# Kernel tuning notes

Measured on AMD Instinct MI355X. Metric: run time of the kernel, lower is better.

## Reference

```python
import jax, jax.numpy as jnp
import numpy as np

N_NODES = 30000
N_EDGES = 480000
C_IN = 256
D_HEAD = 64   # out_channels
N_HEADS = 4
M_FEAT = 30   # nb_random_features
K_GUMBEL = 10
TAU = 0.25


def _linear_init(key, out_f, in_f):
    s = 1.0 / np.sqrt(in_f)
    k1, k2 = jax.random.split(key)
    w = jax.random.uniform(k1, (out_f, in_f), minval=-s, maxval=s, dtype=jnp.float32)
    b = jax.random.uniform(k2, (out_f,), minval=-s, maxval=s, dtype=jnp.float32)
    return w, b


def setup_inputs() -> dict:
    key = jax.random.key(0)
    ks = jax.random.split(key, 8)
    z = jax.random.normal(ks[0], (1, N_NODES, C_IN), dtype=jnp.float32)
    edge_index = jax.random.randint(ks[1], (2, N_EDGES), 0, N_NODES)
    # Gumbel(0,1)/tau noise, matching torch's (-Exp(1).log())/tau
    u = jax.random.uniform(ks[2], (N_NODES, 1, N_HEADS, K_GUMBEL), dtype=jnp.float32,
                           minval=1e-8, maxval=1.0)
    gumbels = -jnp.log(-jnp.log(u)) / TAU
    # Performer orthogonal random-feature projection matrix [M, D]
    rng = np.random.default_rng(0)
    q, _ = np.linalg.qr(rng.standard_normal((D_HEAD, D_HEAD)))
    q = q.T[:M_FEAT]
    mult = np.linalg.norm(rng.standard_normal((M_FEAT, D_HEAD)), axis=1)
    proj = jnp.asarray(np.diag(mult) @ q, dtype=jnp.float32)
    Wq_w, Wq_b = _linear_init(ks[3], N_HEADS * D_HEAD, C_IN)
    Wk_w, Wk_b = _linear_init(ks[4], N_HEADS * D_HEAD, C_IN)
    Wv_w, Wv_b = _linear_init(ks[5], N_HEADS * D_HEAD, C_IN)
    Wo_w, Wo_b = _linear_init(ks[6], D_HEAD, N_HEADS * D_HEAD)
    b = jnp.full((1, N_HEADS), 0.1, dtype=jnp.float32)  # rb_order=1, sigmoid init
    tau = jnp.float32(TAU)
    return {"z": z, "edge_index": edge_index, "tau": tau, "gumbels": gumbels,
            "proj": proj, "Wq_w": Wq_w, "Wq_b": Wq_b, "Wk_w": Wk_w, "Wk_b": Wk_b,
            "Wv_w": Wv_w, "Wv_b": Wv_b, "Wo_w": Wo_w, "Wo_b": Wo_b, "b": b}


def _softmax_kernel_feats(data, proj, is_query):
    # data: [B, N, H, D] -> phi(data): [B, N, H, M]
    dn = 1.0 / jnp.sqrt(jnp.sqrt(jnp.float32(data.shape[-1])))
    data = data * dn
    ratio = 1.0 / jnp.sqrt(jnp.float32(proj.shape[0]))
    dash = jnp.einsum('bnhd,md->bnhm', data, proj)
    diag = jnp.sum(data * data, axis=-1, keepdims=True) * 0.5
    if is_query:
        stab = jnp.max(dash, axis=-1, keepdims=True)
    else:
        stab = jnp.max(dash, axis=(1, 3), keepdims=True)
    return ratio * (jnp.exp(dash - diag - stab) + 1e-6)


def reference(z, edge_index, tau, gumbels, proj, Wq_w, Wq_b, Wk_w, Wk_b,
              Wv_w, Wv_b, Wo_w, Wo_b, b):
    B, N, _ = z.shape
    M, D = proj.shape
    H = Wq_w.shape[0] // D
    query = (z @ Wq_w.T + Wq_b).reshape(B, N, H, D)
    key = (z @ Wk_w.T + Wk_b).reshape(B, N, H, D)
    value = (z @ Wv_w.T + Wv_b).reshape(B, N, H, D)

    inv_sqrt_tau = 1.0 / jnp.sqrt(tau)
    qp = jnp.transpose(_softmax_kernel_feats(query * inv_sqrt_tau, proj, True), (1, 0, 2, 3))   # [N,B,H,M]
    kp = jnp.transpose(_softmax_kernel_feats(key * inv_sqrt_tau, proj, False), (1, 0, 2, 3))    # [N,B,H,M]
    v = jnp.transpose(value, (1, 0, 2, 3))                                                       # [N,B,H,D]

    # Gumbel-perturbed key features: [N,B,H,K,M]
    kg = kp[:, :, :, None, :] * jnp.exp(gumbels)[..., None]
    kvs = jnp.einsum('nbhkm,nbhd->bhkmd', kg, v)
    z_num = jnp.einsum('nbhm,bhkmd->nbhkd', qp, kvs)      # [N,B,H,K,D]
    z_den = jnp.einsum('nbhm,bhkm->nbhk', qp, kg.sum(axis=0))
    z_out = jnp.transpose(jnp.mean(z_num / z_den[..., None], axis=3), (1, 0, 2, 3))  # [B,N,H,D]

    # edge attention weights (for link loss)
    start, end = edge_index[0], edge_index[1]
    edge_num = jnp.transpose(jnp.einsum('ebhm,ebhm->ebh', qp[end], kp[start]), (1, 0, 2))  # [B,E,H]
    attn_norm = jnp.einsum('nbhm,bhm->nbh', qp, kp.sum(axis=0))
    edge_dem = jnp.transpose(attn_norm[end], (1, 0, 2))
    A_weight = edge_num / edge_dem

    # relational bias (rb_order=1, sigmoid), degree-normalized sparse conv over value
    ones_e = jnp.ones(start.shape[0], dtype=jnp.float32)
    d_in = jax.ops.segment_sum(ones_e, end, num_segments=N)
    d_out = jax.ops.segment_sum(ones_e, start, num_segments=N)
    edge_w = jax.nn.sigmoid(b[0])[None, :] * jnp.sqrt((1.0 / d_in[end]) * (1.0 / d_out[start]))[:, None]  # [E,H]
    conv = jax.vmap(lambda vb: jax.ops.segment_sum(vb[start] * edge_w[:, :, None], end,
                                                   num_segments=N))(value)
    z_out = z_out + conv

    z_next = z_out.reshape(B, N, H * D) @ Wo_w.T + Wo_b  # [B,N,D]

    d_norm = 1.0 / d_in[end]
    link_loss = jnp.mean(jnp.log(A_weight) * d_norm[None, :, None])
    return z_next, link_loss
```

## Files before the change

### kernel.cpp

```cpp
#include <hip/hip_runtime.h>
#include <hip/hip_bf16.h>

#define NN 30000
#define NE 480000
#define NH 4
#define DH 64
#define MF 30
#define KG 10
#define RATIO 0.18257418583505536f
#define DNRM  0.35355339059327373f

#define P_WF    0
#define P_BF    196608
#define P_WOF   197376
#define P_WOBF  213760
#define P_BBF   213824
#define P_PROJ  213828
#define P_TAU   215748
#define P_TOTAL 215749

typedef unsigned short u16;
typedef unsigned int   u32;
typedef __attribute__((ext_vector_type(8))) short bf16x8;
typedef __attribute__((ext_vector_type(4))) float f32x4;

__device__ __forceinline__ float u2f(u16 u) { return __uint_as_float(((u32)u) << 16); }
__device__ __forceinline__ u16  f2bf(float f) {
    u32 x = __float_as_uint(f);
    return (u16)((x + 0x7FFFu + ((x >> 16) & 1u)) >> 16);
}
__device__ __forceinline__ u32  encf(float f) { u32 u = __float_as_uint(f); return (u & 0x80000000u) ? ~u : (u | 0x80000000u); }
__device__ __forceinline__ float decf(u32 u)  { return (u & 0x80000000u) ? __uint_as_float(u & 0x7FFFFFFFu) : __uint_as_float(~u); }

__global__ void k_detect(const u16* __restrict__ z, int* __restrict__ flag) {
    if (threadIdx.x == 0 && blockIdx.x == 0) {
        int bad = 0;
        for (int i = 0; i < 256; i += 2) {
            u16 u = z[i];
            int e = (u >> 7) & 0xFF;
            if (u != 0 && !(e >= 100 && e <= 140)) bad++;
        }
        *flag = (bad > 16) ? 1 : 0;
    }
}

__global__ __launch_bounds__(256) void k_cvt_params(
    const void* Wq, const void* Wk, const void* Wv,
    const void* bq, const void* bk, const void* bv,
    const void* Wo, const void* Wob, const void* bb, const void* proj,
    const void* taup, float* __restrict__ params, const int* __restrict__ flag)
{
    int i = blockIdx.x * 256 + threadIdx.x;
    if (i >= P_TOTAL) return;
    int f = *flag;
    if (i == P_TAU) {
        float v = f ? ((const float*)taup)[0] : u2f(((const u16*)taup)[0]);
        if (!(v > 1e-6f && v < 1e6f)) {
            float ff = ((const float*)taup)[0];
            v = (ff > 1e-6f && ff < 1e6f) ? ff : 0.25f;
        }
        params[i] = v;
        return;
    }
    const void* src; int j;
    if      (i < 65536)  { src = Wq;  j = i; }
    else if (i < 131072) { src = Wk;  j = i - 65536; }
    else if (i < 196608) { src = Wv;  j = i - 131072; }
    else if (i < 196864) { src = bq;  j = i - 196608; }
    else if (i < 197120) { src = bk;  j = i - 196864; }
    else if (i < 197376) { src = bv;  j = i - 197120; }
    else if (i < 213760) { src = Wo;  j = i - 197376; }
    else if (i < 213824) { src = Wob; j = i - 213760; }
    else if (i < 213828) { src = bb;  j = i - 213824; }
    else                 { src = proj; j = i - P_PROJ; }
    params[i] = f ? ((const float*)src)[j] : u2f(((const u16*)src)[j]);
}

__global__ __launch_bounds__(256) void k_cvt_w(const float* __restrict__ params,
                                               u16* __restrict__ Wh, u16* __restrict__ Wl)
{
    int i = blockIdx.x * 256 + threadIdx.x;
    float x = params[P_WF + i];
    u16 h = f2bf(x);
    Wh[i] = h;
    Wl[i] = f2bf(x - u2f(h));
}

__global__ __launch_bounds__(256) void k_deg(const int* __restrict__ ei, int* __restrict__ din, int* __restrict__ dout) {
    int e = blockIdx.x * 256 + threadIdx.x;
    if (e >= NE) return;
    atomicAdd(&dout[ei[e]], 1);
    atomicAdd(&din[ei[NE + e]], 1);
}

__global__ __launch_bounds__(256) void k_off(const int* __restrict__ din, int* __restrict__ offn, int* __restrict__ counter) {
    __shared__ int s[256];
    __shared__ int base;
    int tid = threadIdx.x;
    int n = blockIdx.x * 256 + tid;
    int v = (n < NN) ? din[n] : 0;
    s[tid] = v;
    __syncthreads();
    for (int o = 1; o < 256; o <<= 1) {
        int t = (tid >= o) ? s[tid - o] : 0;
        __syncthreads();
        s[tid] += t;
        __syncthreads();
    }
    if (tid == 255) base = atomicAdd(counter, s[255]);
    __syncthreads();
    if (n < NN) offn[n] = base + s[tid] - v;
}

__global__ __launch_bounds__(256) void k_fill(const int* __restrict__ ei, const int* __restrict__ offn,
                                              int* __restrict__ fill, int* __restrict__ csr,
                                              const int* __restrict__ din, const int* __restrict__ dout,
                                              float* __restrict__ wedge) {
    int e = blockIdx.x * 256 + threadIdx.x;
    if (e >= NE) return;
    int s = ei[e], t = ei[NE + e];
    int pos = offn[t] + atomicAdd(&fill[t], 1);
    csr[pos] = s;
    wedge[pos] = rsqrtf((float)din[t] * (float)dout[s]);
}

__global__ __launch_bounds__(256) void k_gemm_feat(
    const void* __restrict__ zv, const float* __restrict__ params, const int* __restrict__ flag,
    const u16* __restrict__ Wh, const u16* __restrict__ Wl,
    u16* __restrict__ V16, float* __restrict__ qp, u16* __restrict__ qp16,
    float* __restrict__ dashK, float* __restrict__ diagK, u32* __restrict__ stab)
{
    __shared__ __align__(16) char AsH[64 * 512];
    __shared__ __align__(16) char AsL[64 * 512];
    __shared__ __align__(16) char BsH[2][64 * 128];
    __shared__ __align__(16) char BsL[2][64 * 128];
    __shared__ float tile[64 * 68];
    __shared__ float projL[30 * 65];
    __shared__ u32 smaxL;

    const int tid = threadIdx.x;
    const int bm = blockIdx.x * 64;
    const int f32 = *flag;
    const int wave = tid >> 6, lane = tid & 63;
    const int wm = wave >> 1, wn = wave & 1;
    const int sr = tid >> 2;
    const int sc = (tid & 3) * 16;

    {
        int zrow = bm + sr;
        if (f32) {
            for (int k0 = 0; k0 < 256; k0 += 64) {
                float x[16];
                if (zrow < NN) {
                    const float4* zp = (const float4*)((const float*)zv + (size_t)zrow * 256 + k0 + sc);
                    #pragma unroll
                    for (int q4 = 0; q4 < 4; ++q4) {
                        float4 v = zp[q4];
                        x[q4 * 4 + 0] = v.x; x[q4 * 4 + 1] = v.y;
                        x[q4 * 4 + 2] = v.z; x[q4 * 4 + 3] = v.w;
                    }
                } else {
                    #pragma unroll
                    for (int j = 0; j < 16; ++j) x[j] = 0.f;
                }
                #pragma unroll
                for (int j8 = 0; j8 < 2; ++j8) {
                    u32 hw[4], lw[4];
                    #pragma unroll
                    for (int p = 0; p < 4; ++p) {
                        float a = x[j8 * 8 + 2 * p], b2 = x[j8 * 8 + 2 * p + 1];
                        u16 ha = f2bf(a), hb = f2bf(b2);
                        hw[p] = (u32)ha | ((u32)hb << 16);
                        u16 la = f2bf(a - u2f(ha)), lb = f2bf(b2 - u2f(hb));
                        lw[p] = (u32)la | ((u32)lb << 16);
                    }
                    int byt = sr * 512 + (((k0 + sc + j8 * 8) * 2) ^ ((sr & 7) << 4));
                    *(uint4*)(AsH + byt) = make_uint4(hw[0], hw[1], hw[2], hw[3]);
                    *(uint4*)(AsL + byt) = make_uint4(lw[0], lw[1], lw[2], lw[3]);
                }
            }
        } else {
            for (int k0 = 0; k0 < 256; k0 += 64) {
                uint4 v0 = make_uint4(0, 0, 0, 0), v1 = v0;
                if (zrow < NN) {
                    const uint4* zp = (const uint4*)((const u16*)zv + (size_t)zrow * 256 + k0 + sc);
                    v0 = zp[0]; v1 = zp[1];
                }
                int byt0 = sr * 512 + (((k0 + sc + 0) * 2) ^ ((sr & 7) << 4));
                int byt1 = sr * 512 + (((k0 + sc + 8) * 2) ^ ((sr & 7) << 4));
                *(uint4*)(AsH + byt0) = v0;
                *(uint4*)(AsH + byt1) = v1;
            }
        }
    }
    for (int i2 = tid; i2 < MF * DH; i2 += 256) projL[(i2 >> 6) * 65 + (i2 & 63)] = params[P_PROJ + i2];

    const float* bfv = params + P_BF;
    float scale = DNRM * rsqrtf(params[P_TAU]);

    for (int bny = 0; bny < 12; ++bny) {
        const int bn = bny * 64;
        f32x4 acc[2][2] = {};
        for (int k0c = 0; k0c < 4; ++k0c) {
            const int k0 = k0c * 64;
            const int p = k0c & 1;
            {
                int byt0 = sr * 128 + (((sc + 0) * 2) ^ ((sr & 7) << 4));
                int byt1 = sr * 128 + (((sc + 8) * 2) ^ ((sr & 7) << 4));
                const uint4* wh4 = (const uint4*)(Wh + (size_t)(bn + sr) * 256 + k0 + sc);
                *(uint4*)(BsH[p] + byt0) = wh4[0];
                *(uint4*)(BsH[p] + byt1) = wh4[1];
                if (f32) {
                    const uint4* wl4 = (const uint4*)(Wl + (size_t)(bn + sr) * 256 + k0 + sc);
                    *(uint4*)(BsL[p] + byt0) = wl4[0];
                    *(uint4*)(BsL[p] + byt1) = wl4[1];
                }
            }
            __syncthreads();
            #pragma unroll
            for (int kk = 0; kk < 2; ++kk) {
                const int kbA = (k0 + kk * 32 + ((lane >> 4) * 8)) * 2;
                const int kbB = (kk * 32 + ((lane >> 4) * 8)) * 2;
                bf16x8 ah[2], bh[2], al[2], bl[2];
                #pragma unroll
                for (int i = 0; i < 2; ++i) {
                    int ar = 32 * wm + 16 * i + (lane & 15);
                    int ab = ar * 512 + (kbA ^ ((ar & 7) << 4));
                    ah[i] = *(const bf16x8*)(AsH + ab);
                    int br = 32 * wn + 16 * i + (lane & 15);
                    int bb2 = br * 128 + (kbB ^ ((br & 7) << 4));
                    bh[i] = *(const bf16x8*)(BsH[p] + bb2);
                    if (f32) {
                        al[i] = *(const bf16x8*)(AsL + ab);
                        bl[i] = *(const bf16x8*)(BsL[p] + bb2);
                    }
                }
                #pragma unroll
                for (int i = 0; i < 2; ++i)
                    #pragma unroll
                    for (int nf = 0; nf < 2; ++nf) {
                        acc[i][nf] = __builtin_amdgcn_mfma_f32_16x16x32_bf16(ah[i], bh[nf], acc[i][nf], 0, 0, 0);
                        if (f32) {
                            acc[i][nf] = __builtin_amdgcn_mfma_f32_16x16x32_bf16(ah[i], bl[nf], acc[i][nf], 0, 0, 0);
                            acc[i][nf] = __builtin_amdgcn_mfma_f32_16x16x32_bf16(al[i], bh[nf], acc[i][nf], 0, 0, 0);
                        }
                    }
            }
        }
        if (bny >= 8) {
            #pragma unroll
            for (int i = 0; i < 2; ++i)
                #pragma unroll
                for (int nf = 0; nf < 2; ++nf) {
                    int col = 32 * wn + 16 * nf + (lane & 15);
                    float bias = bfv[bn + col];
                    #pragma unroll
                    for (int r2 = 0; r2 < 4; ++r2) {
                        int row = 32 * wm + 16 * i + ((lane >> 4) * 4) + r2;
                        tile[row * 68 + col] = acc[i][nf][r2] + bias;
                    }
                }
            __syncthreads();
            for (int i2 = tid; i2 < 4096; i2 += 256) {
                int row = i2 >> 6, col = i2 & 63;
                int nrow = bm + row;
                if (nrow < NN) V16[(size_t)nrow * 256 + (bn - 512) + col] = f2bf(tile[row * 68 + col]);
            }
            continue;
        }

        if (tid == 0) smaxL = 0u;
        #pragma unroll
        for (int i = 0; i < 2; ++i)
            #pragma unroll
            for (int nf = 0; nf < 2; ++nf) {
                int col = 32 * wn + 16 * nf + (lane & 15);
                float bias = bfv[bn + col];
                #pragma unroll
                for (int r2 = 0; r2 < 4; ++r2) {
                    int row = 32 * wm + 16 * i + ((lane >> 4) * 4) + r2;
                    tile[row * 68 + col] = (acc[i][nf][r2] + bias) * scale;
                }
            }
        __syncthreads();

        int r = tid >> 2, q = tid & 3;
        int n = bm + r;
        const float* trow = tile + r * 68;
        float dp = 0.f;
        #pragma unroll
        for (int d = q * 16; d < q * 16 + 16; ++d) dp += trow[d] * trow[d];
        dp += __shfl_xor(dp, 1);
        dp += __shfl_xor(dp, 2);
        float diag = dp * 0.5f;

        float dm[8];
        int nm = 0;
        float lmax = -3.0e38f;
        for (int m = q; m < MF; m += 4) {
            float s = 0.f;
            #pragma unroll
            for (int d = 0; d < DH; ++d) s += trow[d] * projL[m * 65 + d];
            dm[nm++] = s;
            lmax = fmaxf(lmax, s);
        }
        float mx = fmaxf(lmax, __shfl_xor(lmax, 1));
        mx = fmaxf(mx, __shfl_xor(mx, 2));

        if (bny < 4) {
            int h = bny;
            if (n < NN) {
                float* o = qp + ((size_t)n * NH + h) * MF;
                u16* o16 = qp16 + ((size_t)n * NH + h) * 32;
                nm = 0;
                for (int m = q; m < MF; m += 4) {
                    float v = RATIO * (expf(dm[nm++] - diag - mx) + 1e-6f);
                    o[m] = v;
                    o16[m] = f2bf(v);
                }
                if (q == 0) { o16[30] = 0; o16[31] = 0; }
            }
        } else {
            int h = bny - 4;
            if (n < NN) {
                float* o = dashK + ((size_t)n * NH + h) * MF;
                nm = 0;
                for (int m = q; m < MF; m += 4) o[m] = dm[nm++];
                if (q == 0) {
                    diagK[(size_t)n * NH + h] = diag;
                    atomicMax(&smaxL, encf(mx));
                }
            }
            __syncthreads();
            if (tid == 0) atomicMax(&stab[h], smaxL);
        }
    }
}

__global__ __launch_bounds__(256) void k_kp(float* __restrict__ kp, const float* __restrict__ diagK,
                                            const u32* __restrict__ stab, float* __restrict__ kpsum,
                                            u16* __restrict__ kp16)
{
    __shared__ float part[NH * MF];
    __shared__ float stabf[4];
    int tid = threadIdx.x;
    if (tid < NH * MF) part[tid] = 0.f;
    if (tid >= 128 && tid < 132) stabf[tid - 128] = decf(stab[tid - 128]);
    __syncthreads();
    int base = blockIdx.x * 64 * MF;
    for (int i = tid; i < 64 * MF; i += 256) {
        int row = blockIdx.x * 64 + i / MF;
        int m = i - (i / MF) * MF;
        int h = row & 3;
        float v = RATIO * (expf(kp[base + i] - diagK[row] - stabf[h]) + 1e-6f);
        kp[base + i] = v;
        kp16[(size_t)row * 32 + m] = f2bf(v);
        atomicAdd(&part[h * MF + m], v);
    }
    if (tid < 64) {
        int row = blockIdx.x * 64 + tid;
        kp16[(size_t)row * 32 + 30] = 0;
        kp16[(size_t)row * 32 + 31] = 0;
    }
    __syncthreads();
    if (tid < NH * MF) atomicAdd(&kpsum[tid], part[tid]);
}

__global__ __launch_bounds__(256) void k_an(const float* __restrict__ qp, const float* __restrict__ kpsum,
                                            float* __restrict__ an)
{
    __shared__ float kps[NH * MF];
    int tid = threadIdx.x;
    if (tid < NH * MF) kps[tid] = kpsum[tid];
    __syncthreads();
    int idx = blockIdx.x * 256 + tid;
    if (idx >= NN * NH) return;
    int h = idx & 3;
    const float* q = qp + (size_t)idx * MF;
    float s = 0.f;
    #pragma unroll
    for (int m = 0; m < MF; ++m) s += q[m] * kps[h * MF + m];
    an[idx] = s;
}

#define KVS_CHUNKS 50
#define KVS_NPB (NN / KVS_CHUNKS)
__global__ __launch_bounds__(512) void k_kvs(const float* __restrict__ kp, const void* __restrict__ gum,
                                             const u16* __restrict__ V16, const int* __restrict__ flag,
                                             float* __restrict__ Pkvs, float* __restrict__ Pksum)
{
    __shared__ __align__(16) char kgT[320 * 128];
    __shared__ __align__(16) char VT[64 * 128];
    __shared__ float kpT[64][31];
    __shared__ float egT[64][10];
    const int tid = threadIdx.x;
    const int h = blockIdx.y;
    const int chunk = blockIdx.x;
    const int n0 = chunk * KVS_NPB;
    const int f32 = *flag;
    const int wave = tid >> 6, lane = tid & 63;

    float ksacc[5] = {0.f, 0.f, 0.f, 0.f, 0.f};
    f32x4 acc[10] = {};

    for (int t0 = 0; t0 < KVS_NPB; t0 += 64) {
        __syncthreads();
        for (int i = tid; i < 64 * MF; i += 512) {
            int n = i / MF, m = i - (i / MF) * MF;
            kpT[n][m] = (t0 + n < KVS_NPB) ? kp[(size_t)(n0 + t0 + n) * (NH * MF) + h * MF + m] : 0.f;
        }
        for (int i = tid; i < 64 * KG; i += 512) {
            int n = i / KG, k = i - (i / KG) * KG;
            float e = 0.f;
            if (t0 + n < KVS_NPB) {
                size_t gofs = (size_t)(n0 + t0 + n) * (NH * KG) + h * KG + k;
                float g = f32 ? ((const float*)gum)[gofs] : u2f(((const u16*)gum)[gofs]);
                e = expf(g);
            }
            egT[n][k] = e;
        }
        for (int i = tid; i < 64 * 16; i += 512) {
            int n = i >> 4, dq = (i & 15) * 4;
            u32 v0 = 0, v1 = 0;
            if (t0 + n < KVS_NPB) {
                uint2 vv = *(const uint2*)(V16 + (size_t)(n0 + t0 + n) * 256 + h * 64 + dq);
                v0 = vv.x; v1 = vv.y;
            }
            #pragma unroll
            for (int j = 0; j < 4; ++j) {
                u16 val = (u16)(((j < 2) ? v0 : v1) >> ((j & 1) * 16));
                int d = dq + j;
                *(u16*)(VT + d * 128 + ((n * 2) ^ ((d & 7) << 4))) = val;
            }
        }
        __syncthreads();
        #pragma unroll
        for (int it = 0; it < 5; ++it) {
            int idx = tid + it * 512;
            int row = idx >> 3, nc = idx & 7;
            u32 w_[4] = {0u, 0u, 0u, 0u};
            if (row < 300) {
                int k = row / MF, m = row - (row / MF) * MF;
                float s = 0.f;
                #pragma unroll
                for (int p = 0; p < 4; ++p) {
                    int na = nc * 8 + 2 * p, nb = na + 1;
                    u16 ha = f2bf(kpT[na][m] * egT[na][k]);
                    u16 hb = f2bf(kpT[nb][m] * egT[nb][k]);
                    w_[p] = (u32)ha | ((u32)hb << 16);
                    s += u2f(ha) + u2f(hb);
                }
                ksacc[it] += s;
            }
            *(uint4*)(kgT + row * 128 + ((nc * 16) ^ ((row & 7) << 4))) = make_uint4(w_[0], w_[1], w_[2], w_[3]);
        }
        __syncthreads();
        #pragma unroll
        for (int kk = 0; kk < 2; ++kk) {
            const int kb = (kk * 32 + ((lane >> 4) * 8)) * 2;
            #pragma unroll
            for (int i = 0; i < 10; ++i) {
                int ct = wave * 10 + i;
                int kt = ct >> 2, dt = ct & 3;
                int ar = kt * 16 + (lane & 15);
                bf16x8 a = *(const bf16x8*)(kgT + ar * 128 + (kb ^ ((ar & 7) << 4)));
                int br = dt * 16 + (lane & 15);
                bf16x8 b = *(const bf16x8*)(VT + br * 128 + (kb ^ ((br & 7) << 4)));
                acc[i] = __builtin_amdgcn_mfma_f32_16x16x32_bf16(a, b, acc[i], 0, 0, 0);
            }
        }
    }
    #pragma unroll
    for (int i = 0; i < 10; ++i) {
        int ct = wave * 10 + i;
        int kt = ct >> 2, dt = ct & 3;
        int col = dt * 16 + (lane & 15);
        #pragma unroll
        for (int r = 0; r < 4; ++r) {
            int row = kt * 16 + ((lane >> 4) * 4) + r;
            if (row < 300)
                Pkvs[(((size_t)chunk * NH + h) * 300 + row) * 64 + col] = acc[i][r];
        }
    }
    #pragma unroll
    for (int it = 0; it < 5; ++it) {
        float v = ksacc[it];
        v += __shfl_xor(v, 1);
        v += __shfl_xor(v, 2);
        v += __shfl_xor(v, 4);
        int row = (tid + it * 512) >> 3;
        if ((tid & 7) == 0 && row < 300)
            Pksum[chunk * 1200 + h * 300 + row] = v;
    }
}

__global__ __launch_bounds__(256) void k_reduce(const float* __restrict__ Pkvs, const float* __restrict__ Pksum,
                                                float* __restrict__ kvs, float* __restrict__ ksum)
{
    int i = blockIdx.x * 256 + threadIdx.x;
    if (i < NH * KG * MF * DH) {
        float s = 0.f;
        for (int c = 0; c < KVS_CHUNKS; ++c) s += Pkvs[(size_t)c * (NH * 300 * 64) + i];
        kvs[i] = s;
    } else if (i < NH * KG * MF * DH + NH * KG * MF) {
        int j = i - NH * KG * MF * DH;
        float s = 0.f;
        for (int c = 0; c < KVS_CHUNKS; ++c) s += Pksum[c * 1200 + j];
        ksum[j] = s;
    }
}

__global__ __launch_bounds__(256) void k_edge(const int* __restrict__ ei,
                                              const u16* __restrict__ qp16, const u16* __restrict__ kp16,
                                              const float* __restrict__ an,
                                              const int* __restrict__ din, float* __restrict__ lossp)
{
    __shared__ float ls[64];
    int tid = threadIdx.x;
    int eg = tid >> 2, h = tid & 3;
    int e = blockIdx.x * 64 + eg;
    int s = ei[e], t = ei[NE + e];
    const uint4* qv = (const uint4*)(qp16 + ((size_t)t * NH + h) * 32);
    const uint4* kv = (const uint4*)(kp16 + ((size_t)s * NH + h) * 32);
    float num = 0.f;
    #pragma unroll
    for (int c = 0; c < 4; ++c) {
        uint4 a = qv[c], b = kv[c];
        num += u2f((u16)(a.x & 0xFFFF)) * u2f((u16)(b.x & 0xFFFF))
             + u2f((u16)(a.x >> 16))    * u2f((u16)(b.x >> 16))
             + u2f((u16)(a.y & 0xFFFF)) * u2f((u16)(b.y & 0xFFFF))
             + u2f((u16)(a.y >> 16))    * u2f((u16)(b.y >> 16))
             + u2f((u16)(a.z & 0xFFFF)) * u2f((u16)(b.z & 0xFFFF))
             + u2f((u16)(a.z >> 16))    * u2f((u16)(b.z >> 16))
             + u2f((u16)(a.w & 0xFFFF)) * u2f((u16)(b.w & 0xFFFF))
             + u2f((u16)(a.w >> 16))    * u2f((u16)(b.w >> 16));
    }
    float term = logf(num / an[(size_t)t * NH + h]);
    term += __shfl_xor(term, 1);
    term += __shfl_xor(term, 2);
    if (h == 0) ls[eg] = term / (float)din[t];
    __syncthreads();
    if (tid < 64) {
        float v = ls[tid];
        #pragma unroll
        for (int o = 32; o > 0; o >>= 1) v += __shfl_xor(v, o);
        if (tid == 0) atomicAdd(&lossp[blockIdx.x & 1023], v);
    }
}

#define AT_NT 48
__global__ __launch_bounds__(256) void k_attn(
    const float* __restrict__ qp, const float* __restrict__ kvs, const float* __restrict__ ksum,
    u16* __restrict__ zatt)
{
    __shared__ float qpTf[3][NH * 484];
    __shared__ u32   kvbuf[NH * 964];
    __shared__ float rdenL[3][16 * NH * KG];
    u16*   kvL16 = (u16*)kvbuf;
    float* ksL   = (float*)kvbuf;
    int tid = threadIdx.x;
    int n0 = blockIdx.x * AT_NT;

    for (int i = tid; i < AT_NT * NH * MF; i += 256) {
        int j48 = i / (NH * MF); int r = i - j48 * (NH * MF);
        int h = r / MF; int m = r - h * MF;
        qpTf[j48 >> 4][h * 484 + m * 16 + (j48 & 15)] = qp[(size_t)(n0 + j48) * (NH * MF) + r];
    }
    for (int i = tid; i < NH * KG * MF; i += 256) ksL[i] = ksum[i];
    __syncthreads();
    for (int i = tid; i < AT_NT * NH * KG; i += 256) {
        int j48 = i / (NH * KG); int r = i - j48 * (NH * KG);
        int h = r / KG;
        int sub = j48 >> 4, j = j48 & 15;
        float s = 0.f;
        #pragma unroll
        for (int m = 0; m < MF; ++m) s += qpTf[sub][h * 484 + m * 16 + j] * ksL[r * MF + m];
        rdenL[sub][j * (NH * KG) + r] = 1.0f / s;
    }

    const int h  = tid >> 6;
    const int jg = (tid >> 4) & 3;
    const int dg = tid & 15;
    float acc[3][4][4] = {};
    for (int k = 0; k < KG; ++k) {
        __syncthreads();
        for (int i = tid; i < NH * MF * DH; i += 256) {
            int hh = i / (MF * DH); int r = i - hh * (MF * DH);
            kvL16[hh * 1928 + r] = f2bf(kvs[((size_t)(hh * 10 + k) * MF) * DH + r]);
        }
        __syncthreads();
        float ps[3][4][4] = {};
        const u16* kb = kvL16 + h * 1928 + dg * 4;
        const float* qb0 = qpTf[0] + h * 484 + jg * 4;
        const float* qb1 = qpTf[1] + h * 484 + jg * 4;
        const float* qb2 = qpTf[2] + h * 484 + jg * 4;
        #pragma unroll
        for (int m = 0; m < MF; ++m) {
            ushort4 bu = *(const ushort4*)(kb + m * 64);
            float4 b = make_float4(u2f(bu.x), u2f(bu.y), u2f(bu.z), u2f(bu.w));
            float4 a0 = *(const float4*)(qb0 + m * 16);
            float4 a1 = *(const float4*)(qb1 + m * 16);
            float4 a2 = *(const float4*)(qb2 + m * 16);
            ps[0][0][0] += a0.x * b.x; ps[0][0][1] += a0.x * b.y; ps[0][0][2] += a0.x * b.z; ps[0][0][3] += a0.x * b.w;
            ps[0][1][0] += a0.y * b.x; ps[0][1][1] += a0.y * b.y; ps[0][1][2] += a0.y * b.z; ps[0][1][3] += a0.y * b.w;
            ps[0][2][0] += a0.z * b.x; ps[0][2][1] += a0.z * b.y; ps[0][2][2] += a0.z * b.z; ps[0][2][3] += a0.z * b.w;
            ps[0][3][0] += a0.w * b.x; ps[0][3][1] += a0.w * b.y; ps[0][3][2] += a0.w * b.z; ps[0][3][3] += a0.w * b.w;
            ps[1][0][0] += a1.x * b.x; ps[1][0][1] += a1.x * b.y; ps[1][0][2] += a1.x * b.z; ps[1][0][3] += a1.x * b.w;
            ps[1][1][0] += a1.y * b.x; ps[1][1][1] += a1.y * b.y; ps[1][1][2] += a1.y * b.z; ps[1][1][3] += a1.y * b.w;
            ps[1][2][0] += a1.z * b.x; ps[1][2][1] += a1.z * b.y; ps[1][2][2] += a1.z * b.z; ps[1][2][3] += a1.z * b.w;
            ps[1][3][0] += a1.w * b.x; ps[1][3][1] += a1.w * b.y; ps[1][3][2] += a1.w * b.z; ps[1][3][3] += a1.w * b.w;
            ps[2][0][0] += a2.x * b.x; ps[2][0][1] += a2.x * b.y; ps[2][0][2] += a2.x * b.z; ps[2][0][3] += a2.x * b.w;
            ps[2][1][0] += a2.y * b.x; ps[2][1][1] += a2.y * b.y; ps[2][1][2] += a2.y * b.z; ps[2][1][3] += a2.y * b.w;
            ps[2][2][0] += a2.z * b.x; ps[2][2][1] += a2.z * b.y; ps[2][2][2] += a2.z * b.z; ps[2][2][3] += a2.z * b.w;
            ps[2][3][0] += a2.w * b.x; ps[2][3][1] += a2.w * b.y; ps[2][3][2] += a2.w * b.z; ps[2][3][3] += a2.w * b.w;
        }
        #pragma unroll
        for (int sub = 0; sub < 3; ++sub)
            #pragma unroll
            for (int j4 = 0; j4 < 4; ++j4) {
                float rd = rdenL[sub][(jg * 4 + j4) * (NH * KG) + h * KG + k];
                #pragma unroll
                for (int d4 = 0; d4 < 4; ++d4) acc[sub][j4][d4] += ps[sub][j4][d4] * rd;
            }
    }
    #pragma unroll
    for (int sub = 0; sub < 3; ++sub)
        #pragma unroll
        for (int j4 = 0; j4 < 4; ++j4) {
            int n = n0 + sub * 16 + jg * 4 + j4;
            #pragma unroll
            for (int d4 = 0; d4 < 4; ++d4)
                zatt[(size_t)n * 256 + h * 64 + dg * 4 + d4] = f2bf(acc[sub][j4][d4] * (1.0f / KG));
        }
}

__global__ __launch_bounds__(256) void k_gather(
    const u16* __restrict__ zatt, const u16* __restrict__ V16,
    const int* __restrict__ csr, const float* __restrict__ wedge,
    const int* __restrict__ offn, const int* __restrict__ din,
    const float* __restrict__ params, u16* __restrict__ pre)
{
    int tid = threadIdx.x;
    int w = tid >> 6, l = tid & 63;
    int n = blockIdx.x * 4 + w;
    float sigb = 1.f / (1.f + expf(-params[P_BBF + (l >> 4)]));
    int dn = din[n], o0 = offn[n];
    float c0 = 0.f, c1 = 0.f, c2 = 0.f, c3 = 0.f;
    for (int t0 = 0; t0 < dn; t0 += 64) {
        int cnt = min(64, dn - t0);
        int myIdx = 0; float myW = 0.f;
        if (l < cnt) { myIdx = csr[o0 + t0 + l]; myW = wedge[o0 + t0 + l]; }
        int j = 0;
        for (; j + 7 < cnt; j += 8) {
            int   s0 = __shfl(myIdx, j),     s1 = __shfl(myIdx, j + 1);
            int   s2 = __shfl(myIdx, j + 2), s3 = __shfl(myIdx, j + 3);
            int   s4 = __shfl(myIdx, j + 4), s5 = __shfl(myIdx, j + 5);
            int   s6 = __shfl(myIdx, j + 6), s7 = __shfl(myIdx, j + 7);
            float w0 = __shfl(myW, j),     w1 = __shfl(myW, j + 1);
            float w2 = __shfl(myW, j + 2), w3 = __shfl(myW, j + 3);
            float w4 = __shfl(myW, j + 4), w5 = __shfl(myW, j + 5);
            float w6 = __shfl(myW, j + 6), w7 = __shfl(myW, j + 7);
            uint2 a0 = *(const uint2*)(V16 + (size_t)s0 * 256 + l * 4);
            uint2 a1 = *(const uint2*)(V16 + (size_t)s1 * 256 + l * 4);
            uint2 a2 = *(const uint2*)(V16 + (size_t)s2 * 256 + l * 4);
            uint2 a3 = *(const uint2*)(V16 + (size_t)s3 * 256 + l * 4);
            uint2 a4 = *(const uint2*)(V16 + (size_t)s4 * 256 + l * 4);
            uint2 a5 = *(const uint2*)(V16 + (size_t)s5 * 256 + l * 4);
            uint2 a6 = *(const uint2*)(V16 + (size_t)s6 * 256 + l * 4);
            uint2 a7 = *(const uint2*)(V16 + (size_t)s7 * 256 + l * 4);
            c0 += w0 * u2f((u16)(a0.x & 0xFFFF)) + w1 * u2f((u16)(a1.x & 0xFFFF))
                + w2 * u2f((u16)(a2.x & 0xFFFF)) + w3 * u2f((u16)(a3.x & 0xFFFF))
                + w4 * u2f((u16)(a4.x & 0xFFFF)) + w5 * u2f((u16)(a5.x & 0xFFFF))
                + w6 * u2f((u16)(a6.x & 0xFFFF)) + w7 * u2f((u16)(a7.x & 0xFFFF));
            c1 += w0 * u2f((u16)(a0.x >> 16)) + w1 * u2f((u16)(a1.x >> 16))
                + w2 * u2f((u16)(a2.x >> 16)) + w3 * u2f((u16)(a3.x >> 16))
                + w4 * u2f((u16)(a4.x >> 16)) + w5 * u2f((u16)(a5.x >> 16))
                + w6 * u2f((u16)(a6.x >> 16)) + w7 * u2f((u16)(a7.x >> 16));
            c2 += w0 * u2f((u16)(a0.y & 0xFFFF)) + w1 * u2f((u16)(a1.y & 0xFFFF))
                + w2 * u2f((u16)(a2.y & 0xFFFF)) + w3 * u2f((u16)(a3.y & 0xFFFF))
                + w4 * u2f((u16)(a4.y & 0xFFFF)) + w5 * u2f((u16)(a5.y & 0xFFFF))
                + w6 * u2f((u16)(a6.y & 0xFFFF)) + w7 * u2f((u16)(a7.y & 0xFFFF));
            c3 += w0 * u2f((u16)(a0.y >> 16)) + w1 * u2f((u16)(a1.y >> 16))
                + w2 * u2f((u16)(a2.y >> 16)) + w3 * u2f((u16)(a3.y >> 16))
                + w4 * u2f((u16)(a4.y >> 16)) + w5 * u2f((u16)(a5.y >> 16))
                + w6 * u2f((u16)(a6.y >> 16)) + w7 * u2f((u16)(a7.y >> 16));
        }
        for (; j < cnt; ++j) {
            int   s0 = __shfl(myIdx, j);
            float w0 = __shfl(myW, j);
            uint2 a0 = *(const uint2*)(V16 + (size_t)s0 * 256 + l * 4);
            c0 += w0 * u2f((u16)(a0.x & 0xFFFF));
            c1 += w0 * u2f((u16)(a0.x >> 16));
            c2 += w0 * u2f((u16)(a0.y & 0xFFFF));
            c3 += w0 * u2f((u16)(a0.y >> 16));
        }
    }
    uint2 za = *(const uint2*)(zatt + (size_t)n * 256 + l * 4);
    float e0 = u2f((u16)(za.x & 0xFFFF)) + sigb * c0;
    float e1 = u2f((u16)(za.x >> 16))    + sigb * c1;
    float e2 = u2f((u16)(za.y & 0xFFFF)) + sigb * c2;
    float e3 = u2f((u16)(za.y >> 16))    + sigb * c3;
    uint2 r;
    r.x = (u32)f2bf(e0) | ((u32)f2bf(e1) << 16);
    r.y = (u32)f2bf(e2) | ((u32)f2bf(e3) << 16);
    *(uint2*)(pre + (size_t)n * 256 + l * 4) = r;
}

__global__ __launch_bounds__(256) void k_out(
    const u16* __restrict__ pre, const float* __restrict__ params, float* __restrict__ out)
{
    __shared__ __align__(16) char smemc[24576];
    char* As  = smemc;
    char* BsH = smemc + 8192;
    char* BsL = smemc + 16384;
    const int tid = threadIdx.x;
    const int bm = blockIdx.x * 64;
    const int wave = tid >> 6, lane = tid & 63;
    const int wm = wave >> 1, wn = wave & 1;
    const int sr = tid >> 2;
    const int sc = (tid & 3) * 16;

    f32x4 acc[2][2] = {};

    for (int k0 = 0; k0 < 256; k0 += 64) {
        __syncthreads();
        int byt0 = sr * 128 + (((sc + 0) * 2) ^ ((sr & 7) << 4));
        int byt1 = sr * 128 + (((sc + 8) * 2) ^ ((sr & 7) << 4));
        {
            int row = bm + sr;
            uint4 v0 = make_uint4(0, 0, 0, 0), v1 = v0;
            if (row < NN) {
                const uint4* p = (const uint4*)(pre + (size_t)row * 256 + k0 + sc);
                v0 = p[0]; v1 = p[1];
            }
            *(uint4*)(As + byt0) = v0;
            *(uint4*)(As + byt1) = v1;
        }
        {
            float x[16];
            const float4* wr = (const float4*)(params + P_WOF + (size_t)sr * 256 + k0 + sc);
            #pragma unroll
            for (int q4 = 0; q4 < 4; ++q4) {
                float4 v = wr[q4];
                x[q4 * 4 + 0] = v.x; x[q4 * 4 + 1] = v.y;
                x[q4 * 4 + 2] = v.z; x[q4 * 4 + 3] = v.w;
            }
            #pragma unroll
            for (int j8 = 0; j8 < 2; ++j8) {
                u32 hw[4], lw[4];
                #pragma unroll
                for (int p = 0; p < 4; ++p) {
                    float a = x[j8 * 8 + 2 * p], b2 = x[j8 * 8 + 2 * p + 1];
                    u16 ha = f2bf(a), hb = f2bf(b2);
                    hw[p] = (u32)ha | ((u32)hb << 16);
                    u16 la = f2bf(a - u2f(ha)), lb = f2bf(b2 - u2f(hb));
                    lw[p] = (u32)la | ((u32)lb << 16);
                }
                int byt = sr * 128 + (((sc + j8 * 8) * 2) ^ ((sr & 7) << 4));
                *(uint4*)(BsH + byt) = make_uint4(hw[0], hw[1], hw[2], hw[3]);
                *(uint4*)(BsL + byt) = make_uint4(lw[0], lw[1], lw[2], lw[3]);
            }
        }
        __syncthreads();
        #pragma unroll
        for (int kk = 0; kk < 2; ++kk) {
            const int kb = (kk * 32 + ((lane >> 4) * 8)) * 2;
            bf16x8 a[2], bh[2], bl[2];
            #pragma unroll
            for (int i = 0; i < 2; ++i) {
                int ar = 32 * wm + 16 * i + (lane & 15);
                int ab = ar * 128 + (kb ^ ((ar & 7) << 4));
                a[i] = *(const bf16x8*)(As + ab);
                int br = 32 * wn + 16 * i + (lane & 15);
                int bb2 = br * 128 + (kb ^ ((br & 7) << 4));
                bh[i] = *(const bf16x8*)(BsH + bb2);
                bl[i] = *(const bf16x8*)(BsL + bb2);
            }
            #pragma unroll
            for (int i = 0; i < 2; ++i)
                #pragma unroll
                for (int nf = 0; nf < 2; ++nf) {
                    acc[i][nf] = __builtin_amdgcn_mfma_f32_16x16x32_bf16(a[i], bh[nf], acc[i][nf], 0, 0, 0);
                    acc[i][nf] = __builtin_amdgcn_mfma_f32_16x16x32_bf16(a[i], bl[nf], acc[i][nf], 0, 0, 0);
                }
        }
    }
    #pragma unroll
    for (int i = 0; i < 2; ++i)
        #pragma unroll
        for (int nf = 0; nf < 2; ++nf) {
            int col = 32 * wn + 16 * nf + (lane & 15);
            float bias = params[P_WOBF + col];
            #pragma unroll
            for (int r2 = 0; r2 < 4; ++r2) {
                int row = bm + 32 * wm + 16 * i + ((lane >> 4) * 4) + r2;
                if (row < NN) out[(size_t)row * 64 + col] = acc[i][nf][r2] + bias;
            }
        }
}

__global__ __launch_bounds__(256) void k_loss(const float* __restrict__ lossp, float* __restrict__ out) {
    __shared__ float s[256];
    int tid = threadIdx.x;
    float v = 0.f;
    for (int i = tid; i < 1024; i += 256) v += lossp[i];
    s[tid] = v;
    __syncthreads();
    for (int o = 128; o > 0; o >>= 1) {
        if (tid < o) s[tid] += s[tid + o];
        __syncthreads();
    }
    if (tid == 0) out[(size_t)NN * 64] = s[0] / (float)(NE * NH);
}

extern "C" void kernel_launch(void* const* d_in, const int* in_sizes, int n_in,
                              void* d_out, int out_size, void* d_ws, size_t ws_size,
                              hipStream_t stream)
{
    const void* z    = d_in[0];
    const int*  ei   = (const int*)d_in[1];
    const void* taup = d_in[2];
    const void* gum  = d_in[3];
    const void* proj = d_in[4];
    const void* Wq   = d_in[5];
    const void* bq   = d_in[6];
    const void* Wk   = d_in[7];
    const void* bk   = d_in[8];
    const void* Wv   = d_in[9];
    const void* bv   = d_in[10];
    const void* Wo   = d_in[11];
    const void* Wob  = d_in[12];
    const void* bb   = d_in[13];
    float* out = (float*)d_out;

    u16*   V16    = (u16*)d_ws;
    float* qpb    = (float*)d_ws + 3840000;
    float* kpb    = qpb + (size_t)NN * NH * MF;
    float* diagK  = kpb + (size_t)NN * NH * MF;
    float* anb    = diagK + (size_t)NN * NH;
    u16*   zatt   = (u16*)kpb;
    int*   csr    = (int*)(anb + (size_t)NN * NH);
    int*   offn   = csr + NE;
    float* params = (float*)(offn + NN);
    float* kvs    = params + 215752;
    float* ksum   = kvs + NH * KG * MF * DH;
    float* kpsum  = ksum + NH * KG * MF;
    int*   din    = (int*)(kpsum + NH * MF);
    int*   doutd  = din + NN;
    int*   fill   = doutd + NN;
    int*   counter = fill + NN;
    u32*   stab   = (u32*)(counter + 4);
    float* lossp  = (float*)(stab + 4);
    int*   flag   = (int*)(lossp + 1024);
    float* wedge  = (float*)(flag + 4);
    u16*   qp16   = (u16*)(wedge + NE);
    u16*   kp16   = qp16 + (size_t)NN * NH * 32;
    float* Pkvs   = (float*)qp16;
    float* Pksum  = (float*)(kp16 + (size_t)NN * NH * 32);
    u16*   Whb    = kp16;
    u16*   Wlb    = kp16 + 196608;
    u16*   pre    = qp16;
    size_t zero_bytes = (size_t)((char*)(flag + 4) - (char*)kvs);

    hipMemsetAsync(kvs, 0, zero_bytes, stream);

    k_detect<<<dim3(1), dim3(64), 0, stream>>>((const u16*)z, flag);
    k_cvt_params<<<dim3((P_TOTAL + 255) / 256), dim3(256), 0, stream>>>(
        Wq, Wk, Wv, bq, bk, bv, Wo, Wob, bb, proj, taup, params, flag);
    k_cvt_w<<<dim3(768), dim3(256), 0, stream>>>(params, Whb, Wlb);

    k_deg <<<dim3((NE + 255) / 256), dim3(256), 0, stream>>>(ei, din, doutd);
    k_off <<<dim3((NN + 255) / 256), dim3(256), 0, stream>>>(din, offn, counter);
    k_fill<<<dim3((NE + 255) / 256), dim3(256), 0, stream>>>(ei, offn, fill, csr, din, doutd, wedge);
    k_gemm_feat<<<dim3((NN + 63) / 64), dim3(256), 0, stream>>>(
        z, params, flag, Whb, Wlb, V16, qpb, qp16, kpb, diagK, stab);
    k_kp  <<<dim3(NN * NH / 64), dim3(256), 0, stream>>>(kpb, diagK, stab, kpsum, kp16);
    k_an  <<<dim3((NN * NH + 255) / 256), dim3(256), 0, stream>>>(qpb, kpsum, anb);
    k_edge<<<dim3(NE / 64), dim3(256), 0, stream>>>(ei, qp16, kp16, anb, din, lossp);
    k_kvs <<<dim3(KVS_CHUNKS, NH), dim3(512), 0, stream>>>(kpb, gum, V16, flag, Pkvs, Pksum);
    k_reduce<<<dim3((NH * KG * MF * DH + NH * KG * MF + 255) / 256), dim3(256), 0, stream>>>(
        Pkvs, Pksum, kvs, ksum);
    k_attn<<<dim3(NN / AT_NT), dim3(256), 0, stream>>>(qpb, kvs, ksum, zatt);
    k_gather<<<dim3(NN / 4), dim3(256), 0, stream>>>(zatt, V16, csr, wedge, offn, din, params, pre);
    k_out<<<dim3((NN + 63) / 64), dim3(256), 0, stream>>>(pre, params, out);
    k_loss<<<dim3(1), dim3(256), 0, stream>>>(lossp, out);
}
```

Before: 728.3 us.

## Keep A tile in registers and restage per K-chunk to cut LDS footprint

The full 64x256 A tile (hi/lo bf16 split) now lives in 64 VGPRs per thread and is written into a small 64x64 LDS chunk before each K step. The B buffers lose their double-buffering and gain an extra barrier per step. This shrinks shared memory from roughly 96KB to under 60KB so more blocks can fit per CU. The cost is more LDS writes (A is restaged for each of the 12 N blocks), higher register pressure, and an added sync per K chunk.

```diff
diff --git a/kernel.cpp b/kernel.cpp
--- a/kernel.cpp
+++ b/kernel.cpp
@@ -130,10 +130,10 @@
     u16* __restrict__ V16, float* __restrict__ qp, u16* __restrict__ qp16,
     float* __restrict__ dashK, float* __restrict__ diagK, u32* __restrict__ stab)
 {
-    __shared__ __align__(16) char AsH[64 * 512];
-    __shared__ __align__(16) char AsL[64 * 512];
-    __shared__ __align__(16) char BsH[2][64 * 128];
-    __shared__ __align__(16) char BsL[2][64 * 128];
+    __shared__ __align__(16) char AsH[64 * 128];
+    __shared__ __align__(16) char AsL[64 * 128];
+    __shared__ __align__(16) char BsH[64 * 128];
+    __shared__ __align__(16) char BsL[64 * 128];
     __shared__ float tile[64 * 68];
     __shared__ float projL[30 * 65];
     __shared__ u32 smaxL;
@@ -146,13 +146,15 @@
     const int sr = tid >> 2;
     const int sc = (tid & 3) * 16;
 
+    u32 ah[32], al[32];
     {
         int zrow = bm + sr;
         if (f32) {
-            for (int k0 = 0; k0 < 256; k0 += 64) {
+            #pragma unroll
+            for (int c = 0; c < 4; ++c) {
                 float x[16];
                 if (zrow < NN) {
-                    const float4* zp = (const float4*)((const float*)zv + (size_t)zrow * 256 + k0 + sc);
+                    const float4* zp = (const float4*)((const float*)zv + (size_t)zrow * 256 + c * 64 + sc);
                     #pragma unroll
                     for (int q4 = 0; q4 < 4; ++q4) {
                         float4 v = zp[q4];
@@ -164,32 +166,26 @@
                     for (int j = 0; j < 16; ++j) x[j] = 0.f;
                 }
                 #pragma unroll
-                for (int j8 = 0; j8 < 2; ++j8) {
-                    u32 hw[4], lw[4];
+                for (int j8 = 0; j8 < 2; ++j8)
                     #pragma unroll
                     for (int p = 0; p < 4; ++p) {
                         float a = x[j8 * 8 + 2 * p], b2 = x[j8 * 8 + 2 * p + 1];
                         u16 ha = f2bf(a), hb = f2bf(b2);
-                        hw[p] = (u32)ha | ((u32)hb << 16);
+                        ah[c * 8 + j8 * 4 + p] = (u32)ha | ((u32)hb << 16);
                         u16 la = f2bf(a - u2f(ha)), lb = f2bf(b2 - u2f(hb));
-                        lw[p] = (u32)la | ((u32)lb << 16);
+                        al[c * 8 + j8 * 4 + p] = (u32)la | ((u32)lb << 16);
                     }
-                    int byt = sr * 512 + (((k0 + sc + j8 * 8) * 2) ^ ((sr & 7) << 4));
-                    *(uint4*)(AsH + byt) = make_uint4(hw[0], hw[1], hw[2], hw[3]);
-                    *(uint4*)(AsL + byt) = make_uint4(lw[0], lw[1], lw[2], lw[3]);
-                }
             }
         } else {
-            for (int k0 = 0; k0 < 256; k0 += 64) {
+            #pragma unroll
+            for (int c = 0; c < 4; ++c) {
                 uint4 v0 = make_uint4(0, 0, 0, 0), v1 = v0;
                 if (zrow < NN) {
-                    const uint4* zp = (const uint4*)((const u16*)zv + (size_t)zrow * 256 + k0 + sc);
+                    const uint4* zp = (const uint4*)((const u16*)zv + (size_t)zrow * 256 + c * 64 + sc);
                     v0 = zp[0]; v1 = zp[1];
                 }
-                int byt0 = sr * 512 + (((k0 + sc + 0) * 2) ^ ((sr & 7) << 4));
-                int byt1 = sr * 512 + (((k0 + sc + 8) * 2) ^ ((sr & 7) << 4));
-                *(uint4*)(AsH + byt0) = v0;
-                *(uint4*)(AsH + byt1) = v1;
+                ah[c * 8 + 0] = v0.x; ah[c * 8 + 1] = v0.y; ah[c * 8 + 2] = v0.z; ah[c * 8 + 3] = v0.w;
+                ah[c * 8 + 4] = v1.x; ah[c * 8 + 5] = v1.y; ah[c * 8 + 6] = v1.z; ah[c * 8 + 7] = v1.w;
             }
         }
     }
@@ -197,52 +193,58 @@
 
     const float* bfv = params + P_BF;
     float scale = DNRM * rsqrtf(params[P_TAU]);
+    const int byt0 = sr * 128 + (((sc + 0) * 2) ^ ((sr & 7) << 4));
+    const int byt1 = sr * 128 + (((sc + 8) * 2) ^ ((sr & 7) << 4));
 
     for (int bny = 0; bny < 12; ++bny) {
         const int bn = bny * 64;
         f32x4 acc[2][2] = {};
+        #pragma unroll
         for (int k0c = 0; k0c < 4; ++k0c) {
             const int k0 = k0c * 64;
-            const int p = k0c & 1;
+            __syncthreads();
+            *(uint4*)(AsH + byt0) = make_uint4(ah[k0c * 8 + 0], ah[k0c * 8 + 1], ah[k0c * 8 + 2], ah[k0c * 8 + 3]);
+            *(uint4*)(AsH + byt1) = make_uint4(ah[k0c * 8 + 4], ah[k0c * 8 + 5], ah[k0c * 8 + 6], ah[k0c * 8 + 7]);
+            if (f32) {
+                *(uint4*)(AsL + byt0) = make_uint4(al[k0c * 8 + 0], al[k0c * 8 + 1], al[k0c * 8 + 2], al[k0c * 8 + 3]);
+                *(uint4*)(AsL + byt1) = make_uint4(al[k0c * 8 + 4], al[k0c * 8 + 5], al[k0c * 8 + 6], al[k0c * 8 + 7]);
+            }
             {
-                int byt0 = sr * 128 + (((sc + 0) * 2) ^ ((sr & 7) << 4));
-                int byt1 = sr * 128 + (((sc + 8) * 2) ^ ((sr & 7) << 4));
                 const uint4* wh4 = (const uint4*)(Wh + (size_t)(bn + sr) * 256 + k0 + sc);
-                *(uint4*)(BsH[p] + byt0) = wh4[0];
-                *(uint4*)(BsH[p] + byt1) = wh4[1];
+                *(uint4*)(BsH + byt0) = wh4[0];
+                *(uint4*)(BsH + byt1) = wh4[1];
                 if (f32) {
                     const uint4* wl4 = (const uint4*)(Wl + (size_t)(bn + sr) * 256 + k0 + sc);
-                    *(uint4*)(BsL[p] + byt0) = wl4[0];
-                    *(uint4*)(BsL[p] + byt1) = wl4[1];
+                    *(uint4*)(BsL + byt0) = wl4[0];
+                    *(uint4*)(BsL + byt1) = wl4[1];
                 }
             }
             __syncthreads();
             #pragma unroll
             for (int kk = 0; kk < 2; ++kk) {
-                const int kbA = (k0 + kk * 32 + ((lane >> 4) * 8)) * 2;
-                const int kbB = (kk * 32 + ((lane >> 4) * 8)) * 2;
-                bf16x8 ah[2], bh[2], al[2], bl[2];
+                const int kb = (kk * 32 + ((lane >> 4) * 8)) * 2;
+                bf16x8 ahf[2], bhf[2], alf[2], blf[2];
                 #pragma unroll
                 for (int i = 0; i < 2; ++i) {
                     int ar = 32 * wm + 16 * i + (lane & 15);
-                    int ab = ar * 512 + (kbA ^ ((ar & 7) << 4));
-                    ah[i] = *(const bf16x8*)(AsH + ab);
+                    int ab = ar * 128 + (kb ^ ((ar & 7) << 4));
+                    ahf[i] = *(const bf16x8*)(AsH + ab);
                     int br = 32 * wn + 16 * i + (lane & 15);
-                    int bb2 = br * 128 + (kbB ^ ((br & 7) << 4));
-                    bh[i] = *(const bf16x8*)(BsH[p] + bb2);
+                    int bb2 = br * 128 + (kb ^ ((br & 7) << 4));
+                    bhf[i] = *(const bf16x8*)(BsH + bb2);
                     if (f32) {
-                        al[i] = *(const bf16x8*)(AsL + ab);
-                        bl[i] = *(const bf16x8*)(BsL[p] + bb2);
+                        alf[i] = *(const bf16x8*)(AsL + ab);
+                        blf[i] = *(const bf16x8*)(BsL + bb2);
                     }
                 }
                 #pragma unroll
                 for (int i = 0; i < 2; ++i)
                     #pragma unroll
                     for (int nf = 0; nf < 2; ++nf) {
-                        acc[i][nf] = __builtin_amdgcn_mfma_f32_16x16x32_bf16(ah[i], bh[nf], acc[i][nf], 0, 0, 0);
+                        acc[i][nf] = __builtin_amdgcn_mfma_f32_16x16x32_bf16(ahf[i], bhf[nf], acc[i][nf], 0, 0, 0);
                         if (f32) {
-                            acc[i][nf] = __builtin_amdgcn_mfma_f32_16x16x32_bf16(ah[i], bl[nf], acc[i][nf], 0, 0, 0);
-                            acc[i][nf] = __builtin_amdgcn_mfma_f32_16x16x32_bf16(al[i], bh[nf], acc[i][nf], 0, 0, 0);
+                            acc[i][nf] = __builtin_amdgcn_mfma_f32_16x16x32_bf16(ahf[i], blf[nf], acc[i][nf], 0, 0, 0);
+                            acc[i][nf] = __builtin_amdgcn_mfma_f32_16x16x32_bf16(alf[i], bhf[nf], acc[i][nf], 0, 0, 0);
                         }
                     }
             }
```

Result: faster. 675.7 us, median of 3 (-7.2%).
